# Performance work log

Measured on AMD Instinct MI355X. Metric: run time of the kernel, lower is better.

The kernel has to match this reference:

```python
import jax, jax.numpy as jnp
import numpy as np

N_NODES = 100000
N_EDGES = 1600000
IN_CH = 128
HIDDEN = 64
HEADS = 4
C = HIDDEN // HEADS  # per-head channels = 16
NEG_SLOPE = 0.2  # PyG GATConv default leaky_relu slope


def setup_inputs() -> dict:
    key = jax.random.key(0)
    ks = jax.random.split(key, 12)
    x = jax.random.normal(ks[0], (N_NODES, IN_CH), dtype=jnp.float32)
    edge_index = jax.random.randint(ks[1], (2, N_EDGES), 0, N_NODES, dtype=jnp.int64)
    s = 0.1
    params = {
        'w1': jax.random.normal(ks[2], (HIDDEN, IN_CH), dtype=jnp.float32) * s,
        'a_src1': jax.random.normal(ks[3], (HEADS, C), dtype=jnp.float32) * s,
        'a_dst1': jax.random.normal(ks[4], (HEADS, C), dtype=jnp.float32) * s,
        'b1': jax.random.normal(ks[5], (HIDDEN,), dtype=jnp.float32) * s,
        'w2': jax.random.normal(ks[6], (HIDDEN, HIDDEN), dtype=jnp.float32) * s,
        'a_src2': jax.random.normal(ks[7], (HEADS, C), dtype=jnp.float32) * s,
        'a_dst2': jax.random.normal(ks[8], (HEADS, C), dtype=jnp.float32) * s,
        'b2': jax.random.normal(ks[9], (HIDDEN,), dtype=jnp.float32) * s,
        'fc_w': jax.random.normal(ks[10], (1, HIDDEN), dtype=jnp.float32) * s,
        'fc_b': jax.random.normal(ks[11], (1,), dtype=jnp.float32) * s,
    }
    return {'x': x, 'edge_index': edge_index, **params}


def _gat_layer(x, src, dst, W, a_src, a_dst, b):
    # x: [N, F_in]; src/dst: [E'] (self-loops already appended)
    N = x.shape[0]
    h = (x @ W.T).reshape(N, HEADS, C)                      # [N, H, C]
    e_src = jnp.einsum('nhc,hc->nh', h, a_src)              # [N, H]
    e_dst = jnp.einsum('nhc,hc->nh', h, a_dst)              # [N, H]
    alpha = jax.nn.leaky_relu(e_src[src] + e_dst[dst], NEG_SLOPE)  # [E', H]
    # segment softmax over incoming edges of each dst node
    amax = jax.ops.segment_max(alpha, dst, num_segments=N)  # [N, H]
    alpha = jnp.exp(alpha - amax[dst])
    denom = jax.ops.segment_sum(alpha, dst, num_segments=N)
    alpha = alpha / (denom[dst] + 1e-16)
    msg = h[src] * alpha[:, :, None]                        # [E', H, C]
    out = jax.ops.segment_sum(msg, dst, num_segments=N)     # [N, H, C]
    return out.reshape(N, HEADS * C) + b


def _forward(x, edge_index, w1, a_src1, a_dst1, b1, w2, a_src2, a_dst2, b2, fc_w, fc_b):
    N = x.shape[0]
    loops = jnp.arange(N, dtype=edge_index.dtype)
    src = jnp.concatenate([edge_index[0], loops])  # PyG GATConv add_self_loops=True
    dst = jnp.concatenate([edge_index[1], loops])
    x = jax.nn.elu(_gat_layer(x, src, dst, w1, a_src1, a_dst1, b1))
    x = jax.nn.elu(_gat_layer(x, src, dst, w2, a_src2, a_dst2, b2))
    return x @ fc_w.T + fc_b  # [N, 1]


def reference(x, edge_index, w1, a_src1, a_dst1, b1, w2, a_src2, a_dst2, b2, fc_w, fc_b):
    return _forward(x, edge_index, w1, a_src1, a_dst1, b1, w2, a_src2, a_dst2, b2, fc_w, fc_b)
```

## Files before the change

kernel.cpp:

```cpp
#include <hip/hip_runtime.h>
#include <hip/hip_fp16.h>
#include <math.h>

#define NEG_SLOPE 0.2f
#define BSH 8
#define CAPB 6144

__device__ __forceinline__ float lrelu(float x) { return x > 0.f ? x : NEG_SLOPE * x; }

using half4 = __attribute__((ext_vector_type(4))) _Float16;
using half8 = __attribute__((ext_vector_type(8))) _Float16;
using f32x4 = __attribute__((ext_vector_type(4))) float;

template <typename TIn>
__device__ __forceinline__ float4 ld4(const TIn* p);
template <>
__device__ __forceinline__ float4 ld4<float>(const float* p) { return *(const float4*)p; }
template <>
__device__ __forceinline__ float4 ld4<_Float16>(const _Float16* p) {
    half4 v = *(const half4*)p;
    return make_float4((float)v[0], (float)v[1], (float)v[2], (float)v[3]);
}

template <int K, typename TIn>
__device__ __forceinline__ void gemm_mfma_body(const TIn* __restrict__ x,
                                               const float* __restrict__ W,
                                               const float* __restrict__ a_src,
                                               const float* __restrict__ a_dst,
                                               unsigned short* __restrict__ h_f16,
                                               float* __restrict__ es,
                                               float* __restrict__ ed,
                                               int N, int bid, _Float16* sm) {
    constexpr int KP = K + 8;
    _Float16* xs = sm;
    _Float16* ws = sm + 64 * KP;
    const int tid = threadIdx.x;
    const int n0 = bid * 64;

    constexpr int KV = K / 4;
    for (int idx = tid; idx < 64 * KV; idx += 256) {
        int r = idx / KV, kq = idx - r * KV;
        int n = n0 + r;
        float4 v = (n < N) ? ld4<TIn>(x + (size_t)n * K + kq * 4)
                           : make_float4(0.f, 0.f, 0.f, 0.f);
        half4 hv = {(_Float16)v.x, (_Float16)v.y, (_Float16)v.z, (_Float16)v.w};
        *(half4*)&xs[r * KP + kq * 4] = hv;
        float4 wv = *(const float4*)(W + (size_t)r * K + kq * 4);
        half4 wh = {(_Float16)wv.x, (_Float16)wv.y, (_Float16)wv.z, (_Float16)wv.w};
        *(half4*)&ws[r * KP + kq * 4] = wh;
    }
    __syncthreads();

    const int wv_ = tid >> 6, lane = tid & 63;
    const int lrow = lane & 15, g = lane >> 4;
    f32x4 acc0 = {0.f, 0.f, 0.f, 0.f}, acc1 = acc0, acc2 = acc0, acc3 = acc0;
#pragma unroll
    for (int ks = 0; ks < K / 32; ++ks) {
        const int ko = ks * 32 + g * 8;
        half8 af = *(const half8*)&xs[(wv_ * 16 + lrow) * KP + ko];
        half8 b0 = *(const half8*)&ws[(lrow) * KP + ko];
        half8 b1 = *(const half8*)&ws[(16 + lrow) * KP + ko];
        half8 b2 = *(const half8*)&ws[(32 + lrow) * KP + ko];
        half8 b3 = *(const half8*)&ws[(48 + lrow) * KP + ko];
        acc0 = __builtin_amdgcn_mfma_f32_16x16x32_f16(af, b0, acc0, 0, 0, 0);
        acc1 = __builtin_amdgcn_mfma_f32_16x16x32_f16(af, b1, acc1, 0, 0, 0);
        acc2 = __builtin_amdgcn_mfma_f32_16x16x32_f16(af, b2, acc2, 0, 0, 0);
        acc3 = __builtin_amdgcn_mfma_f32_16x16x32_f16(af, b3, acc3, 0, 0, 0);
    }
    __syncthreads();

    _Float16* ht = sm;
#pragma unroll
    for (int reg = 0; reg < 4; ++reg) {
        int r = wv_ * 16 + g * 4 + reg;
        ht[r * 72 +      lrow] = (_Float16)acc0[reg];
        ht[r * 72 + 16 + lrow] = (_Float16)acc1[reg];
        ht[r * 72 + 32 + lrow] = (_Float16)acc2[reg];
        ht[r * 72 + 48 + lrow] = (_Float16)acc3[reg];
    }
    __syncthreads();

    {
        int nl = tid >> 2, hd = tid & 3;
        half8 hA = *(const half8*)&ht[nl * 72 + hd * 16];
        half8 hB = *(const half8*)&ht[nl * 72 + hd * 16 + 8];
        const float4 s0 = *(const float4*)(a_src + hd * 16);
        const float4 s1 = *(const float4*)(a_src + hd * 16 + 4);
        const float4 s2 = *(const float4*)(a_src + hd * 16 + 8);
        const float4 s3 = *(const float4*)(a_src + hd * 16 + 12);
        const float4 d0 = *(const float4*)(a_dst + hd * 16);
        const float4 d1 = *(const float4*)(a_dst + hd * 16 + 4);
        const float4 d2 = *(const float4*)(a_dst + hd * 16 + 8);
        const float4 d3 = *(const float4*)(a_dst + hd * 16 + 12);
        float e1 = (float)hA[0]*s0.x + (float)hA[1]*s0.y + (float)hA[2]*s0.z + (float)hA[3]*s0.w
                 + (float)hA[4]*s1.x + (float)hA[5]*s1.y + (float)hA[6]*s1.z + (float)hA[7]*s1.w
                 + (float)hB[0]*s2.x + (float)hB[1]*s2.y + (float)hB[2]*s2.z + (float)hB[3]*s2.w
                 + (float)hB[4]*s3.x + (float)hB[5]*s3.y + (float)hB[6]*s3.z + (float)hB[7]*s3.w;
        float e2 = (float)hA[0]*d0.x + (float)hA[1]*d0.y + (float)hA[2]*d0.z + (float)hA[3]*d0.w
                 + (float)hA[4]*d1.x + (float)hA[5]*d1.y + (float)hA[6]*d1.z + (float)hA[7]*d1.w
                 + (float)hB[0]*d2.x + (float)hB[1]*d2.y + (float)hB[2]*d2.z + (float)hB[3]*d2.w
                 + (float)hB[4]*d3.x + (float)hB[5]*d3.y + (float)hB[6]*d3.z + (float)hB[7]*d3.w;
        int n = n0 + nl;
        if (n < N) {
            es[(size_t)n * 4 + hd] = e1;
            ed[(size_t)n * 4 + hd] = e2;
        }
    }
    for (int idx = tid; idx < 512; idx += 256) {
        int r = idx >> 3, c8 = (idx & 7) << 3;
        if (n0 + r < N)
            *(uint4*)(h_f16 + (size_t)(n0 + r) * 64 + c8) = *(const uint4*)&ht[r * 72 + c8];
    }
}

template <int K>
__global__ __launch_bounds__(256) void gemm1_hist(const float* __restrict__ x,
                                                  const float* __restrict__ W,
                                                  const float* __restrict__ a_src,
                                                  const float* __restrict__ a_dst,
                                                  unsigned short* __restrict__ h_f16,
                                                  float* __restrict__ es,
                                                  float* __restrict__ ed, int N,
                                                  const int* __restrict__ dst,
                                                  int* __restrict__ hist_g,
                                                  int E, int Etot, int NBUCK, int nIter,
                                                  int NH) {
    __shared__ _Float16 sm[2 * 64 * (K + 8)];
    if ((int)blockIdx.x < NH) {
        int* hist = (int*)sm;
        int blk = blockIdx.x, tid = threadIdx.x;
        for (int i = tid; i < NBUCK; i += 256) hist[i] = 0;
        __syncthreads();
        int base = blk * nIter * 256;
        for (int i = 0; i < nIter; ++i) {
            int e = base + i * 256 + tid;
            if (e < Etot) {
                int d = (e < E) ? dst[e] : e - E;
                atomicAdd(&hist[d >> BSH], 1);
            }
        }
        __syncthreads();
        for (int i = tid; i < NBUCK; i += 256) hist_g[(size_t)blk * NBUCK + i] = hist[i];
        return;
    }
    gemm_mfma_body<K, float>(x, W, a_src, a_dst, h_f16, es, ed, N, blockIdx.x - NH, sm);
}

template <int K, typename TIn>
__global__ __launch_bounds__(256) void gemm_mfma(const TIn* __restrict__ x,
                                                 const float* __restrict__ W,
                                                 const float* __restrict__ a_src,
                                                 const float* __restrict__ a_dst,
                                                 unsigned short* __restrict__ h_f16,
                                                 float* __restrict__ es,
                                                 float* __restrict__ ed, int N) {
    __shared__ _Float16 sm[2 * 64 * (K + 8)];
    gemm_mfma_body<K, TIn>(x, W, a_src, a_dst, h_f16, es, ed, N, blockIdx.x, sm);
}

__global__ __launch_bounds__(256) void bucket_scan_blocks(int* __restrict__ hist_g,
                                                          int* __restrict__ tot,
                                                          int NBUCK, int NBLK) {
    __shared__ int s[256];
    int b = blockIdx.x, tid = threadIdx.x;
    int v = (tid < NBLK) ? hist_g[(size_t)tid * NBUCK + b] : 0;
    s[tid] = v; __syncthreads();
#pragma unroll
    for (int off = 1; off < 256; off <<= 1) {
        int t = (tid >= off) ? s[tid - off] : 0;
        __syncthreads();
        s[tid] += t;
        __syncthreads();
    }
    if (tid < NBLK) hist_g[(size_t)tid * NBUCK + b] = s[tid] - v;
    if (tid == 255) tot[b] = s[255];
}

__device__ __forceinline__ void local_tot_scan(const int* __restrict__ tot, int* sv, int NBUCK) {
    int tid = threadIdx.x;
    sv[tid]       = (tid < NBUCK)       ? tot[tid]       : 0;
    sv[tid + 256] = (tid + 256 < NBUCK) ? tot[tid + 256] : 0;
    __syncthreads();
#pragma unroll
    for (int off = 1; off < 512; off <<= 1) {
        int a1 = (tid >= off) ? sv[tid - off] : 0;
        int a2 = (tid + 256 >= off) ? sv[tid + 256 - off] : 0;
        __syncthreads();
        sv[tid] += a1; sv[tid + 256] += a2;
        __syncthreads();
    }
}

__global__ __launch_bounds__(256) void bucket_scatter(const int* __restrict__ src,
                                                      const int* __restrict__ dst,
                                                      const int* __restrict__ hist_g,
                                                      const int* __restrict__ tot,
                                                      unsigned int* __restrict__ bbuf,
                                                      int E, int Etot, int NBUCK, int nIter) {
    __shared__ int sv[512];
    __shared__ int lcur[512];
    int blk = blockIdx.x, tid = threadIdx.x;
    local_tot_scan(tot, sv, NBUCK);
    for (int i = tid; i < NBUCK; i += 256)
        lcur[i] = (sv[i] - tot[i]) + hist_g[(size_t)blk * NBUCK + i];
    __syncthreads();
    int base = blk * nIter * 256;
    for (int i = 0; i < nIter; ++i) {
        int e = base + i * 256 + tid;
        if (e >= Etot) continue;
        int s, d;
        if (e < E) { s = src[e]; d = dst[e]; } else { s = d = e - E; }
        int pos = atomicAdd(&lcur[d >> BSH], 1);
        bbuf[pos] = (unsigned)s | ((unsigned)(d & ((1 << BSH) - 1)) << 24);
    }
}

__global__ __launch_bounds__(256) void bucket_build(const unsigned int* __restrict__ bbuf,
                                                    const int* __restrict__ tot,
                                                    int* __restrict__ col,
                                                    int* __restrict__ offs,
                                                    int N, int NBUCK, int Etot) {
    __shared__ int sv[512];
    __shared__ int cnt[256], lcur[256], s[256];
    __shared__ int ordered[CAPB];
    int b = blockIdx.x, tid = threadIdx.x;
    local_tot_scan(tot, sv, NBUCK);
    const int t  = tot[b];
    const int bb = sv[b] - t;
    const int n0 = b << BSH;
    if (b == 0 && tid == 0) offs[N] = Etot;
    cnt[tid] = 0;
    __syncthreads();
    for (int i = tid; i < t; i += 256) {
        unsigned v = bbuf[bb + i];
        atomicAdd(&cnt[v >> 24], 1);
    }
    __syncthreads();
    int c = cnt[tid];
    s[tid] = c; __syncthreads();
#pragma unroll
    for (int off = 1; off < 256; off <<= 1) {
        int tt = (tid >= off) ? s[tid - off] : 0;
        __syncthreads();
        s[tid] += tt;
        __syncthreads();
    }
    int ex = s[tid] - c;
    lcur[tid] = ex;
    if (n0 + tid < N) offs[n0 + tid] = bb + ex;
    __syncthreads();
    if (t <= CAPB) {
        for (int i = tid; i < t; i += 256) {
            unsigned v = bbuf[bb + i];
            int pos = atomicAdd(&lcur[v >> 24], 1);
            ordered[pos] = (int)(v & 0xFFFFFFu);
        }
        __syncthreads();
        for (int i = tid; i < t; i += 256) col[bb + i] = ordered[i];
    } else {
        for (int i = tid; i < t; i += 256) {
            unsigned v = bbuf[bb + i];
            int pos = atomicAdd(&lcur[v >> 24], 1);
            col[bb + pos] = (int)(v & 0xFFFFFFu);
        }
    }
}

template <int D>
__device__ __forceinline__ void batchD(int myCol, int cm1, int cnt64, int eslot,
                                       int co, int hd, float edv,
                                       const float* __restrict__ es,
                                       const unsigned short* __restrict__ h_f16,
                                       float* acc, float& l) {
    int   sidx[D];
    float ev[D];
    uint4 hv[D];
#pragma unroll
    for (int d = 0; d < D; ++d)
        sidx[d] = __shfl(myCol, min(eslot + 8 * d, cm1), 64);
#pragma unroll
    for (int d = 0; d < D; ++d)
        ev[d] = es[(size_t)sidx[d] * 4 + hd];
#pragma unroll
    for (int d = 0; d < D; ++d)
        hv[d] = *(const uint4*)(h_f16 + (size_t)sidx[d] * 64 + co * 8);
    float p[D];
#pragma unroll
    for (int d = 0; d < D; ++d)
        p[d] = (eslot + 8 * d < cnt64) ? __expf(lrelu(ev[d] + edv)) : 0.f;
#pragma unroll
    for (int d = 0; d < D; ++d) {
        union { uint4 u; __half h[8]; } u;
        u.u = hv[d];
        acc[0] += p[d] * __half2float(u.h[0]); acc[1] += p[d] * __half2float(u.h[1]);
        acc[2] += p[d] * __half2float(u.h[2]); acc[3] += p[d] * __half2float(u.h[3]);
        acc[4] += p[d] * __half2float(u.h[4]); acc[5] += p[d] * __half2float(u.h[5]);
        acc[6] += p[d] * __half2float(u.h[6]); acc[7] += p[d] * __half2float(u.h[7]);
        l += p[d];
    }
}

template <bool FINAL>
__global__ __launch_bounds__(256) void gat_gather32(const int* __restrict__ offs,
                                                    const int* __restrict__ col,
                                                    const float* __restrict__ es,
                                                    const float* __restrict__ ed,
                                                    const unsigned short* __restrict__ h_f16,
                                                    const float* __restrict__ b,
                                                    const float* __restrict__ fcw,
                                                    const float* __restrict__ fcb,
                                                    float* __restrict__ xo,
                                                    unsigned short* __restrict__ xo_h,
                                                    int N) {
    int w = (blockIdx.x * 256 + threadIdx.x) >> 6;
    if (w >= N) return;
    const int lane = threadIdx.x & 63;
    const int eslot = lane >> 3, co = lane & 7, hd = co >> 1;
    const int beg = offs[w];
    const int cnt = offs[w + 1] - beg;
    const float edv = ed[(size_t)w * 4 + hd];

    const int cnt64 = min(cnt, 64);
    const int cm1 = cnt64 - 1;
    int myCol = col[beg + min(lane, cm1)];

    float acc[8] = {0.f, 0.f, 0.f, 0.f, 0.f, 0.f, 0.f, 0.f};
    float l = 0.f;

    if (cnt64 <= 8) {
        batchD<1>(myCol, cm1, cnt64, eslot, co, hd, edv, es, h_f16, acc, l);
    } else if (cnt64 <= 16) {
        batchD<2>(myCol, cm1, cnt64, eslot, co, hd, edv, es, h_f16, acc, l);
    } else if (cnt64 <= 24) {
        batchD<3>(myCol, cm1, cnt64, eslot, co, hd, edv, es, h_f16, acc, l);
    } else {
        batchD<4>(myCol, cm1, cnt64, eslot, co, hd, edv, es, h_f16, acc, l);
        for (int j = 32; j < cnt64; j += 8) {
            int k = j + eslot;
            bool valid = k < cnt64;
            int s = __shfl(myCol, min(k, cm1), 64);
            float a = es[(size_t)s * 4 + hd] + edv;
            float p = valid ? __expf(lrelu(a)) : 0.f;
            union { uint4 u; __half h[8]; } hv;
            hv.u = *(const uint4*)(h_f16 + (size_t)s * 64 + co * 8);
            acc[0] += p * __half2float(hv.h[0]); acc[1] += p * __half2float(hv.h[1]);
            acc[2] += p * __half2float(hv.h[2]); acc[3] += p * __half2float(hv.h[3]);
            acc[4] += p * __half2float(hv.h[4]); acc[5] += p * __half2float(hv.h[5]);
            acc[6] += p * __half2float(hv.h[6]); acc[7] += p * __half2float(hv.h[7]);
            l += p;
        }
        for (int j = 64; j < cnt; j += 8) {
            int k = j + eslot;
            bool valid = k < cnt;
            int s = valid ? col[beg + k] : 0;
            float a = es[(size_t)s * 4 + hd] + edv;
            float p = valid ? __expf(lrelu(a)) : 0.f;
            union { uint4 u; __half h[8]; } hv;
            hv.u = *(const uint4*)(h_f16 + (size_t)s * 64 + co * 8);
            acc[0] += p * __half2float(hv.h[0]); acc[1] += p * __half2float(hv.h[1]);
            acc[2] += p * __half2float(hv.h[2]); acc[3] += p * __half2float(hv.h[3]);
            acc[4] += p * __half2float(hv.h[4]); acc[5] += p * __half2float(hv.h[5]);
            acc[6] += p * __half2float(hv.h[6]); acc[7] += p * __half2float(hv.h[7]);
            l += p;
        }
    }

#pragma unroll
    for (int m = 8; m <= 32; m <<= 1) {
#pragma unroll
        for (int q = 0; q < 8; ++q) acc[q] += __shfl_xor(acc[q], m, 64);
        l += __shfl_xor(l, m, 64);
    }
    const float inv = 1.f / (l + 1e-16f);
    const float4 bv0 = *(const float4*)(b + co * 8);
    const float4 bv1 = *(const float4*)(b + co * 8 + 4);
    float v0 = acc[0] * inv + bv0.x, v1 = acc[1] * inv + bv0.y;
    float v2 = acc[2] * inv + bv0.z, v3 = acc[3] * inv + bv0.w;
    float v4 = acc[4] * inv + bv1.x, v5 = acc[5] * inv + bv1.y;
    float v6 = acc[6] * inv + bv1.z, v7 = acc[7] * inv + bv1.w;
    v0 = v0 > 0.f ? v0 : __expf(v0) - 1.f;
    v1 = v1 > 0.f ? v1 : __expf(v1) - 1.f;
    v2 = v2 > 0.f ? v2 : __expf(v2) - 1.f;
    v3 = v3 > 0.f ? v3 : __expf(v3) - 1.f;
    v4 = v4 > 0.f ? v4 : __expf(v4) - 1.f;
    v5 = v5 > 0.f ? v5 : __expf(v5) - 1.f;
    v6 = v6 > 0.f ? v6 : __expf(v6) - 1.f;
    v7 = v7 > 0.f ? v7 : __expf(v7) - 1.f;
    if (FINAL) {
        const float4 fw0 = *(const float4*)(fcw + co * 8);
        const float4 fw1 = *(const float4*)(fcw + co * 8 + 4);
        float t = v0 * fw0.x + v1 * fw0.y + v2 * fw0.z + v3 * fw0.w +
                  v4 * fw1.x + v5 * fw1.y + v6 * fw1.z + v7 * fw1.w;
#pragma unroll
        for (int m = 1; m <= 4; m <<= 1) t += __shfl_xor(t, m, 64);
        if (lane == 0) xo[w] = t + fcb[0];
    } else {
        if (lane < 8) {
            unsigned p0u = (unsigned)__half_as_ushort(__float2half_rn(v0)) |
                           ((unsigned)__half_as_ushort(__float2half_rn(v1)) << 16);
            unsigned p1u = (unsigned)__half_as_ushort(__float2half_rn(v2)) |
                           ((unsigned)__half_as_ushort(__float2half_rn(v3)) << 16);
            unsigned p2u = (unsigned)__half_as_ushort(__float2half_rn(v4)) |
                           ((unsigned)__half_as_ushort(__float2half_rn(v5)) << 16);
            unsigned p3u = (unsigned)__half_as_ushort(__float2half_rn(v6)) |
                           ((unsigned)__half_as_ushort(__float2half_rn(v7)) << 16);
            *(uint4*)(xo_h + (size_t)w * 64 + co * 8) = make_uint4(p0u, p1u, p2u, p3u);
        }
    }
}

extern "C" void kernel_launch(void* const* d_in, const int* in_sizes, int n_in,
                              void* d_out, int out_size, void* d_ws, size_t ws_size,
                              hipStream_t stream) {
    const float* x   = (const float*)d_in[0];
    const int*   ei  = (const int*)d_in[1];
    const float* w1  = (const float*)d_in[2];
    const float* as1 = (const float*)d_in[3];
    const float* ad1 = (const float*)d_in[4];
    const float* b1  = (const float*)d_in[5];
    const float* w2  = (const float*)d_in[6];
    const float* as2 = (const float*)d_in[7];
    const float* ad2 = (const float*)d_in[8];
    const float* b2  = (const float*)d_in[9];
    const float* fcw = (const float*)d_in[10];
    const float* fcb = (const float*)d_in[11];
    float* out = (float*)d_out;

    const int N = in_sizes[0] / 128;
    const int E = in_sizes[1] / 2;
    const int Etot = E + N;
    const int* src = ei;
    const int* dst = ei + E;

    const int NBUCK = (N + 255) >> BSH;
    int CHe = 8192;
    while ((Etot + CHe - 1) / CHe > 256) CHe *= 2;
    const int NBLK = (Etot + CHe - 1) / CHe;
    const int nIter = CHe / 256;

    char* p = (char*)d_ws;
    unsigned short* h_f16 = (unsigned short*)p;  p += (size_t)N * 64 * 2;
    unsigned short* x2    = (unsigned short*)p;  p += (size_t)N * 64 * 2;
    float* es    = (float*)p;  p += (size_t)N * 4 * 4;
    float* ed    = (float*)p;  p += (size_t)N * 4 * 4;
    int* offs    = (int*)p;    p += (size_t)(N + 1) * 4;
    int* tot     = (int*)p;    p += (size_t)NBUCK * 4;
    int* hist_g  = (int*)p;    p += (size_t)NBLK * NBUCK * 4;
    int* col     = (int*)p;    p += (size_t)Etot * 4;
    unsigned int* bbuf = (unsigned int*)p;  p += (size_t)Etot * 4;

    dim3 blk(256);
    const int gN64t = (N + 63) / 64;
    const int gW    = (N * 64 + 255) / 256;

    gemm1_hist<128><<<NBLK + gN64t, blk, 0, stream>>>(x, w1, as1, ad1, h_f16, es, ed, N,
                                                      dst, hist_g, E, Etot, NBUCK, nIter, NBLK);
    bucket_scan_blocks<<<NBUCK, blk, 0, stream>>>(hist_g, tot, NBUCK, NBLK);
    bucket_scatter<<<NBLK, blk, 0, stream>>>(src, dst, hist_g, tot, bbuf, E, Etot, NBUCK, nIter);
    bucket_build<<<NBUCK, blk, 0, stream>>>(bbuf, tot, col, offs, N, NBUCK, Etot);

    gat_gather32<false><<<gW, blk, 0, stream>>>(offs, col, es, ed, h_f16, b1,
                                                nullptr, nullptr, nullptr, x2, N);
    gemm_mfma<64, _Float16><<<gN64t, blk, 0, stream>>>((const _Float16*)x2, w2, as2, ad2,
                                                       h_f16, es, ed, N);
    gat_gather32<true><<<gW, blk, 0, stream>>>(offs, col, es, ed, h_f16, b2,
                                               fcw, fcb, out, nullptr, N);
}
```

Measured before the change: 160.1 us.

## Process two destination nodes per wavefront in GAT gather kernels

The gather kernel now assigns two destination nodes to each 64-lane wavefront, 32 lanes per node, with 4 edge slots per node instead of 8. Average in-degree is about 17, so a full wavefront per node left many lanes idle. This halves the wavefront count and raises lane utilisation. In exchange, the batch size is chosen from the larger degree of the pair, so divergence between the two halves can waste work, and high-degree nodes now take more serial iterations.

Result: faster. 150.6 us (median of 3 runs) (-6.0%).

```diff
diff --git a/kernel.cpp b/kernel.cpp
--- a/kernel.cpp
+++ b/kernel.cpp
@@ -267,17 +267,17 @@
 }
 
 template <int D>
-__device__ __forceinline__ void batchD(int myCol, int cm1, int cnt64, int eslot,
-                                       int co, int hd, float edv,
-                                       const float* __restrict__ es,
-                                       const unsigned short* __restrict__ h_f16,
-                                       float* acc, float& l) {
+__device__ __forceinline__ void batch2n(int myCol, int cm1, int cnt32, int half,
+                                        int eslot, int co, int hd, float edv,
+                                        const float* __restrict__ es,
+                                        const unsigned short* __restrict__ h_f16,
+                                        float* acc, float& l) {
     int   sidx[D];
     float ev[D];
     uint4 hv[D];
 #pragma unroll
     for (int d = 0; d < D; ++d)
-        sidx[d] = __shfl(myCol, min(eslot + 8 * d, cm1), 64);
+        sidx[d] = __shfl(myCol, (half << 5) + min(eslot + 4 * d, cm1), 64);
 #pragma unroll
     for (int d = 0; d < D; ++d)
         ev[d] = es[(size_t)sidx[d] * 4 + hd];
@@ -287,7 +287,7 @@
     float p[D];
 #pragma unroll
     for (int d = 0; d < D; ++d)
-        p[d] = (eslot + 8 * d < cnt64) ? __expf(lrelu(ev[d] + edv)) : 0.f;
+        p[d] = (eslot + 4 * d < cnt32) ? __expf(lrelu(ev[d] + edv)) : 0.f;
 #pragma unroll
     for (int d = 0; d < D; ++d) {
         union { uint4 u; __half h[8]; } u;
@@ -301,7 +301,7 @@
 }
 
 template <bool FINAL>
-__global__ __launch_bounds__(256) void gat_gather32(const int* __restrict__ offs,
+__global__ __launch_bounds__(256) void gat_gather2n(const int* __restrict__ offs,
                                                     const int* __restrict__ col,
                                                     const float* __restrict__ es,
                                                     const float* __restrict__ ed,
@@ -312,44 +312,35 @@
                                                     float* __restrict__ xo,
                                                     unsigned short* __restrict__ xo_h,
                                                     int N) {
-    int w = (blockIdx.x * 256 + threadIdx.x) >> 6;
-    if (w >= N) return;
+    const int pair = (blockIdx.x * 256 + threadIdx.x) >> 6;
     const int lane = threadIdx.x & 63;
-    const int eslot = lane >> 3, co = lane & 7, hd = co >> 1;
-    const int beg = offs[w];
-    const int cnt = offs[w + 1] - beg;
-    const float edv = ed[(size_t)w * 4 + hd];
-
-    const int cnt64 = min(cnt, 64);
-    const int cm1 = cnt64 - 1;
-    int myCol = col[beg + min(lane, cm1)];
+    const int half = lane >> 5, ll = lane & 31;
+    const int eslot = ll >> 3, co = ll & 7, hd = co >> 1;
+    const int w = pair * 2 + half;
+    const bool vnode = w < N;
+
+    int beg = 0, cnt = 1;
+    if (vnode) { beg = offs[w]; cnt = offs[w + 1] - beg; }
+    const float edv = vnode ? ed[(size_t)w * 4 + hd] : 0.f;
+
+    const int cnt32 = min(cnt, 32);
+    const int cm1 = cnt32 - 1;
+    int myCol = col[beg + min(ll, cm1)];
+    int mcnt = max(cnt, __shfl_xor(cnt, 32, 64));
 
     float acc[8] = {0.f, 0.f, 0.f, 0.f, 0.f, 0.f, 0.f, 0.f};
     float l = 0.f;
 
-    if (cnt64 <= 8) {
-        batchD<1>(myCol, cm1, cnt64, eslot, co, hd, edv, es, h_f16, acc, l);
-    } else if (cnt64 <= 16) {
-        batchD<2>(myCol, cm1, cnt64, eslot, co, hd, edv, es, h_f16, acc, l);
-    } else if (cnt64 <= 24) {
-        batchD<3>(myCol, cm1, cnt64, eslot, co, hd, edv, es, h_f16, acc, l);
+    const int mcnt32 = min(mcnt, 32);
+    if (mcnt32 <= 8) {
+        batch2n<2>(myCol, cm1, cnt32, half, eslot, co, hd, edv, es, h_f16, acc, l);
+    } else if (mcnt32 <= 16) {
+        batch2n<4>(myCol, cm1, cnt32, half, eslot, co, hd, edv, es, h_f16, acc, l);
+    } else if (mcnt32 <= 24) {
+        batch2n<6>(myCol, cm1, cnt32, half, eslot, co, hd, edv, es, h_f16, acc, l);
     } else {
-        batchD<4>(myCol, cm1, cnt64, eslot, co, hd, edv, es, h_f16, acc, l);
-        for (int j = 32; j < cnt64; j += 8) {
-            int k = j + eslot;
-            bool valid = k < cnt64;
-            int s = __shfl(myCol, min(k, cm1), 64);
-            float a = es[(size_t)s * 4 + hd] + edv;
-            float p = valid ? __expf(lrelu(a)) : 0.f;
-            union { uint4 u; __half h[8]; } hv;
-            hv.u = *(const uint4*)(h_f16 + (size_t)s * 64 + co * 8);
-            acc[0] += p * __half2float(hv.h[0]); acc[1] += p * __half2float(hv.h[1]);
-            acc[2] += p * __half2float(hv.h[2]); acc[3] += p * __half2float(hv.h[3]);
-            acc[4] += p * __half2float(hv.h[4]); acc[5] += p * __half2float(hv.h[5]);
-            acc[6] += p * __half2float(hv.h[6]); acc[7] += p * __half2float(hv.h[7]);
-            l += p;
-        }
-        for (int j = 64; j < cnt; j += 8) {
+        batch2n<8>(myCol, cm1, cnt32, half, eslot, co, hd, edv, es, h_f16, acc, l);
+        for (int j = 32; j < mcnt; j += 4) {
             int k = j + eslot;
             bool valid = k < cnt;
             int s = valid ? col[beg + k] : 0;
@@ -366,7 +357,7 @@
     }
 
 #pragma unroll
-    for (int m = 8; m <= 32; m <<= 1) {
+    for (int m = 8; m <= 16; m <<= 1) {
 #pragma unroll
         for (int q = 0; q < 8; ++q) acc[q] += __shfl_xor(acc[q], m, 64);
         l += __shfl_xor(l, m, 64);
@@ -393,9 +384,9 @@
                   v4 * fw1.x + v5 * fw1.y + v6 * fw1.z + v7 * fw1.w;
 #pragma unroll
         for (int m = 1; m <= 4; m <<= 1) t += __shfl_xor(t, m, 64);
-        if (lane == 0) xo[w] = t + fcb[0];
+        if (ll == 0 && vnode) xo[w] = t + fcb[0];
     } else {
-        if (lane < 8) {
+        if (ll < 8 && vnode) {
             unsigned p0u = (unsigned)__half_as_ushort(__float2half_rn(v0)) |
                            ((unsigned)__half_as_ushort(__float2half_rn(v1)) << 16);
             unsigned p1u = (unsigned)__half_as_ushort(__float2half_rn(v2)) |
@@ -451,7 +442,8 @@
 
     dim3 blk(256);
     const int gN64t = (N + 63) / 64;
-    const int gW    = (N * 64 + 255) / 256;
+    const int nPair = (N + 1) / 2;
+    const int gW2   = (nPair * 64 + 255) / 256;
 
     gemm1_hist<128><<<NBLK + gN64t, blk, 0, stream>>>(x, w1, as1, ad1, h_f16, es, ed, N,
                                                       dst, hist_g, E, Etot, NBUCK, nIter, NBLK);
@@ -459,10 +451,10 @@
     bucket_scatter<<<NBLK, blk, 0, stream>>>(src, dst, hist_g, tot, bbuf, E, Etot, NBUCK, nIter);
     bucket_build<<<NBUCK, blk, 0, stream>>>(bbuf, tot, col, offs, N, NBUCK, Etot);
 
-    gat_gather32<false><<<gW, blk, 0, stream>>>(offs, col, es, ed, h_f16, b1,
-                                                nullptr, nullptr, nullptr, x2, N);
+    gat_gather2n<false><<<gW2, blk, 0, stream>>>(offs, col, es, ed, h_f16, b1,
+                                                 nullptr, nullptr, nullptr, x2, N);
     gemm_mfma<64, _Float16><<<gN64t, blk, 0, stream>>>((const _Float16*)x2, w2, as2, ad2,
                                                        h_f16, es, ed, N);
-    gat_gather32<true><<<gW, blk, 0, stream>>>(offs, col, es, ed, h_f16, b2,
-                                               fcw, fcb, out, nullptr, N);
-}
+    gat_gather2n<true><<<gW2, blk, 0, stream>>>(offs, col, es, ed, h_f16, b2,
+                                                fcw, fcb, out, nullptr, N);
+}
```
